# Kernel optimization log

Hardware: AMD Instinct MI355X
Metric: run time of the kernel (lower is better)

The kernel has to match this reference:

```python
import jax, jax.numpy as jnp
import numpy as np

D_MODEL = 2048
N_HEADS = 16
D_HEAD = 128
B = 2
S = 2048


def setup_inputs() -> dict:
    key = jax.random.key(0)
    ks = jax.random.split(key, 9)
    sc_in = 1.0 / np.sqrt(D_MODEL)
    sc_hd = 1.0 / np.sqrt(N_HEADS * D_HEAD)
    return {
        "x": jax.random.normal(ks[0], (B, S, D_MODEL), dtype=jnp.float32),
        "Wq": jax.random.normal(ks[1], (D_MODEL, N_HEADS * D_HEAD), dtype=jnp.float32) * sc_in,
        "bq": jax.random.normal(ks[2], (N_HEADS * D_HEAD,), dtype=jnp.float32) * 0.01,
        "Wk": jax.random.normal(ks[3], (D_MODEL, N_HEADS * D_HEAD), dtype=jnp.float32) * sc_in,
        "bk": jax.random.normal(ks[4], (N_HEADS * D_HEAD,), dtype=jnp.float32) * 0.01,
        "Wv": jax.random.normal(ks[5], (D_MODEL, N_HEADS * D_HEAD), dtype=jnp.float32) * sc_in,
        "bv": jax.random.normal(ks[6], (N_HEADS * D_HEAD,), dtype=jnp.float32) * 0.01,
        "Wo": jax.random.normal(ks[7], (N_HEADS * D_HEAD, D_MODEL), dtype=jnp.float32) * sc_hd,
        "bo": jax.random.normal(ks[8], (D_MODEL,), dtype=jnp.float32) * 0.01,
    }


def reference(x, Wq, bq, Wk, bk, Wv, bv, Wo, bo):
    b, s, _ = x.shape
    # projections -> [b, s, h, d] -> [b, h, s, d]
    q = (x @ Wq + bq).reshape(b, s, N_HEADS, D_HEAD).transpose(0, 2, 1, 3)
    k = (x @ Wk + bk).reshape(b, s, N_HEADS, D_HEAD).transpose(0, 2, 1, 3)
    v = (x @ Wv + bv).reshape(b, s, N_HEADS, D_HEAD).transpose(0, 2, 1, 3)
    scale = 1.0 / jnp.sqrt(jnp.asarray(D_HEAD, dtype=x.dtype))
    scores = jnp.einsum("bhsd,bhtd->bhst", q, k) * scale  # [b,h,s,s]
    causal = jnp.triu(jnp.ones((s, s), dtype=bool), k=1)
    scores = jnp.where(causal, jnp.asarray(-jnp.inf, dtype=scores.dtype), scores)
    attn = jax.nn.softmax(scores, axis=-1)
    ctx = jnp.einsum("bhst,bhtd->bhsd", attn, v)  # [b,h,s,d]
    ctx = ctx.transpose(0, 2, 1, 3).reshape(b, s, N_HEADS * D_HEAD)
    return ctx @ Wo + bo
```

## Files before the change

kernel.cpp:

```cpp
#include <hip/hip_runtime.h>
#include <hip/hip_bf16.h>
#include <stdint.h>

#define S_LEN  2048
#define DMODEL 2048
#define NHEADS 16
#define DHEAD  128
#define NBATCH 2
#define MROWS  (NBATCH * S_LEN)

typedef __bf16 bf16_t;
typedef __bf16 bf16x8 __attribute__((ext_vector_type(8)));
typedef float  f32x4  __attribute__((ext_vector_type(4)));
typedef float  f32x16 __attribute__((ext_vector_type(16)));

#define MFMA_BF16(A, B, C) __builtin_amdgcn_mfma_f32_16x16x32_bf16((A), (B), (C), 0, 0, 0)
#define MFMA32(A, B, C)    __builtin_amdgcn_mfma_f32_32x32x16_bf16((A), (B), (C), 0, 0, 0)

__device__ __forceinline__ void gload_lds16(const void* g, void* l) {
  __builtin_amdgcn_global_load_lds(
      (__attribute__((address_space(1))) uint32_t*)(uintptr_t)g,
      (__attribute__((address_space(3))) uint32_t*)l,
      16, 0, 0);
}

__device__ __forceinline__ unsigned pk2(float lo, float hi) {
  const unsigned short a = __builtin_bit_cast(unsigned short, (bf16_t)lo);
  const unsigned short b = __builtin_bit_cast(unsigned short, (bf16_t)hi);
  return (unsigned)a | ((unsigned)b << 16);
}

__global__ __launch_bounds__(256) void cast_kernel(const float* __restrict__ X,
                                                   bf16_t* __restrict__ Xb) {
  const int i = blockIdx.x * 256 + threadIdx.x;
  const f32x4 a = ((const f32x4*)X)[2 * i];
  const f32x4 b = ((const f32x4*)X)[2 * i + 1];
  bf16x8 o;
#pragma unroll
  for (int j = 0; j < 4; ++j) { o[j] = (bf16_t)a[j]; o[j + 4] = (bf16_t)b[j]; }
  ((bf16x8*)Xb)[i] = o;
}

__global__ __launch_bounds__(256) void transpose_cast(
    const float* __restrict__ W0, const float* __restrict__ W1,
    const float* __restrict__ W2, const float* __restrict__ W3,
    bf16_t* __restrict__ T0, bf16_t* __restrict__ T1,
    bf16_t* __restrict__ T2, bf16_t* __restrict__ T3) {
  const float* W; bf16_t* T;
  switch (blockIdx.z) {
    case 0:  W = W0; T = T0; break;
    case 1:  W = W1; T = T1; break;
    case 2:  W = W2; T = T2; break;
    default: W = W3; T = T3; break;
  }
  __shared__ float tile[64][65];
  const int r0 = blockIdx.y * 64;
  const int c0 = blockIdx.x * 64;
  const int tx = threadIdx.x & 63;
  const int ty = threadIdx.x >> 6;
#pragma unroll
  for (int i = 0; i < 16; ++i) {
    const int r = ty + i * 4;
    tile[r][tx] = W[(size_t)(r0 + r) * DMODEL + c0 + tx];
  }
  __syncthreads();
#pragma unroll
  for (int i = 0; i < 16; ++i) {
    const int r = ty + i * 4;
    T[(size_t)(c0 + r) * DMODEL + r0 + tx] = (bf16_t)tile[tx][r];
  }
}

__global__ __launch_bounds__(256) void transpose_v(const bf16_t* __restrict__ V,
                                                   bf16_t* __restrict__ VT) {
  __shared__ bf16_t tile[64 * 64];
  const int bh = blockIdx.z;
  const int s0 = blockIdx.x * 64;
  const int d0 = blockIdx.y * 64;
  const bf16_t* src = V + ((size_t)bh * S_LEN + s0) * DHEAD + d0;
#pragma unroll
  for (int i = 0; i < 2; ++i) {
    const int v = threadIdx.x + i * 256;
    const int r = v >> 3, ch = v & 7;
    *(bf16x8*)&tile[r * 64 + ((ch ^ ((r >> 3) & 7)) << 3)] =
        *(const bf16x8*)(src + (size_t)r * DHEAD + ch * 8);
  }
  __syncthreads();
  bf16_t* dst = VT + ((size_t)bh * DHEAD + d0) * S_LEN + s0;
#pragma unroll
  for (int i = 0; i < 2; ++i) {
    const int v = threadIdx.x + i * 256;
    const int d = v >> 3, j = v & 7;
    bf16x8 o;
#pragma unroll
    for (int e = 0; e < 8; ++e) {
      const int row = j * 8 + e;
      o[e] = tile[row * 64 + (((d >> 3) ^ j) << 3) + (d & 7)];
    }
    *(bf16x8*)(dst + (size_t)d * S_LEN + j * 8) = o;
  }
}

__global__ __launch_bounds__(512, 2) void gemm_qkv(
    const bf16_t* __restrict__ Xb,
    const bf16_t* __restrict__ WqT, const bf16_t* __restrict__ WkT,
    const bf16_t* __restrict__ WvT,
    const float* __restrict__ bq, const float* __restrict__ bk,
    const float* __restrict__ bv,
    bf16_t* __restrict__ Qg, bf16_t* __restrict__ Kg, bf16_t* __restrict__ Vg) {
  __shared__ __align__(16) char lds[2 * 65536];

  const int tid  = threadIdx.x;
  const int lane = tid & 63;
  const int w    = tid >> 6;
  const int g    = lane >> 4;
  const int l16  = lane & 15;
  const int wm   = w >> 2;
  const int wn   = w & 3;
  const int NTILES = DMODEL / 64;

  const int bid = blockIdx.x;
  const int wg  = (bid & 7) * 48 + (bid >> 3);
  const int mi  = wg / 24;
  const int ni  = wg % 24;
  const int z0  = ni >> 3;
  const bf16_t* Bt = (z0 == 0) ? WqT : (z0 == 1) ? WkT : WvT;
  const bf16_t* Abase = Xb + (size_t)mi * 256 * DMODEL;
  const bf16_t* Bbase = Bt + (size_t)(ni & 7) * 256 * DMODEL;

  f32x4 acc[8][4];
#pragma unroll
  for (int i = 0; i < 8; ++i)
#pragma unroll
    for (int j = 0; j < 4; ++j) acc[i][j] = (f32x4){0.f, 0.f, 0.f, 0.f};

  auto stage = [&](int tile, int mat, int half) {
    if (tile >= NTILES) return;
    const bf16_t* gb = (mat ? Bbase : Abase) + (size_t)(half * 128) * DMODEL + tile * 64;
    char* unit = lds + (tile & 1) * 65536 + mat * 32768 + half * 16384;
#pragma unroll
    for (int jj = 0; jj < 2; ++jj) {
      const int c   = jj * 512 + tid;
      const int row = c >> 3;
      const int ch  = c & 7;
      gload_lds16(gb + (size_t)row * DMODEL + ((ch ^ (row & 7)) << 3),
                  unit + (jj * 512 + (tid & ~63)) * 16);
    }
  };

  stage(0, 0, 0); stage(0, 0, 1); stage(0, 1, 0); stage(0, 1, 1);
  stage(1, 0, 0); stage(1, 0, 1);
  asm volatile("s_waitcnt vmcnt(4)" ::: "memory");
  __builtin_amdgcn_s_barrier();

  for (int t = 0; t < NTILES; ++t) {
    const char* cbA = lds + (t & 1) * 65536;
    const char* cbB = cbA + 32768;
    bf16x8 af[4][2], bf0[2][2], bf1[2][2];

#pragma unroll
    for (int i = 0; i < 4; ++i) {
      const int row = wm * 128 + i * 16 + l16;
#pragma unroll
      for (int ks = 0; ks < 2; ++ks)
        af[i][ks] = *(const bf16x8*)(cbA + row * 128 + ((((ks << 2) | g) ^ (row & 7)) << 4));
    }
#pragma unroll
    for (int j = 0; j < 2; ++j) {
      const int row = wn * 64 + j * 16 + l16;
#pragma unroll
      for (int ks = 0; ks < 2; ++ks)
        bf0[j][ks] = *(const bf16x8*)(cbB + row * 128 + ((((ks << 2) | g) ^ (row & 7)) << 4));
    }
    stage(t + 1, 1, 0);
    __builtin_amdgcn_s_barrier();
    asm volatile("s_waitcnt lgkmcnt(0)" ::: "memory");
    __builtin_amdgcn_s_setprio(1);
#pragma unroll
    for (int i = 0; i < 4; ++i)
#pragma unroll
      for (int j = 0; j < 2; ++j) {
        acc[i][j] = MFMA_BF16(af[i][0], bf0[j][0], acc[i][j]);
        acc[i][j] = MFMA_BF16(af[i][1], bf0[j][1], acc[i][j]);
      }
    __builtin_amdgcn_s_setprio(0);
    __builtin_amdgcn_s_barrier();

#pragma unroll
    for (int j = 0; j < 2; ++j) {
      const int row = wn * 64 + (j + 2) * 16 + l16;
#pragma unroll
      for (int ks = 0; ks < 2; ++ks)
        bf1[j][ks] = *(const bf16x8*)(cbB + row * 128 + ((((ks << 2) | g) ^ (row & 7)) << 4));
    }
    stage(t + 1, 1, 1);
    __builtin_amdgcn_s_barrier();
    asm volatile("s_waitcnt lgkmcnt(0)" ::: "memory");
    __builtin_amdgcn_s_setprio(1);
#pragma unroll
    for (int i = 0; i < 4; ++i)
#pragma unroll
      for (int j = 0; j < 2; ++j) {
        acc[i][j + 2] = MFMA_BF16(af[i][0], bf1[j][0], acc[i][j + 2]);
        acc[i][j + 2] = MFMA_BF16(af[i][1], bf1[j][1], acc[i][j + 2]);
      }
    __builtin_amdgcn_s_setprio(0);
    __builtin_amdgcn_s_barrier();

#pragma unroll
    for (int i = 0; i < 4; ++i) {
      const int row = wm * 128 + (i + 4) * 16 + l16;
#pragma unroll
      for (int ks = 0; ks < 2; ++ks)
        af[i][ks] = *(const bf16x8*)(cbA + row * 128 + ((((ks << 2) | g) ^ (row & 7)) << 4));
    }
    __builtin_amdgcn_s_barrier();
    asm volatile("s_waitcnt lgkmcnt(0)" ::: "memory");
    __builtin_amdgcn_s_setprio(1);
#pragma unroll
    for (int i = 0; i < 4; ++i)
#pragma unroll
      for (int j = 0; j < 2; ++j) {
        acc[i + 4][j + 2] = MFMA_BF16(af[i][0], bf1[j][0], acc[i + 4][j + 2]);
        acc[i + 4][j + 2] = MFMA_BF16(af[i][1], bf1[j][1], acc[i + 4][j + 2]);
      }
    __builtin_amdgcn_s_setprio(0);
    __builtin_amdgcn_s_barrier();

    stage(t + 2, 0, 0); stage(t + 2, 0, 1);
    __builtin_amdgcn_s_setprio(1);
#pragma unroll
    for (int i = 0; i < 4; ++i)
#pragma unroll
      for (int j = 0; j < 2; ++j) {
        acc[i + 4][j] = MFMA_BF16(af[i][0], bf0[j][0], acc[i + 4][j]);
        acc[i + 4][j] = MFMA_BF16(af[i][1], bf0[j][1], acc[i + 4][j]);
      }
    __builtin_amdgcn_s_setprio(0);
    if (t < NTILES - 2) { asm volatile("s_waitcnt vmcnt(4)" ::: "memory"); }
    else                { asm volatile("s_waitcnt vmcnt(0)" ::: "memory"); }
    __builtin_amdgcn_s_barrier();
  }

  const float* bias = (z0 == 0) ? bq : (z0 == 1) ? bk : bv;
  bf16_t* outb      = (z0 == 0) ? Qg : (z0 == 1) ? Kg : Vg;
#pragma unroll
  for (int i = 0; i < 8; ++i) {
#pragma unroll
    for (int j = 0; j < 4; ++j) {
      const int nloc = (ni & 7) * 256 + wn * 64 + j * 16 + l16;
      const float bb = bias[nloc];
      const int h = nloc >> 7, d = nloc & (DHEAD - 1);
#pragma unroll
      for (int r = 0; r < 4; ++r) {
        const int mrow = mi * 256 + wm * 128 + i * 16 + g * 4 + r;
        const int b = mrow >> 11, s = mrow & (S_LEN - 1);
        outb[((size_t)(b * NHEADS + h) * S_LEN + s) * DHEAD + d] =
            (bf16_t)(acc[i][j][r] + bb);
      }
    }
  }
}

template <int MODE>
__device__ __forceinline__ void gemm8_body(const bf16_t* __restrict__ A,
                                           const bf16_t* __restrict__ Bt,
                                           const float* __restrict__ bias,
                                           void* __restrict__ out) {
  __shared__ __align__(16) char lds8[2 * 49152];
  const int tid  = threadIdx.x;
  const int lane = tid & 63;
  const int w    = tid >> 6;
  const int g    = lane >> 4;
  const int l16  = lane & 15;
  const int wm   = w >> 2;
  const int wn   = w & 3;
  const int m0   = blockIdx.y * 128;
  const int n0   = blockIdx.x * 256;

  f32x4 acc[4][4];
#pragma unroll
  for (int i = 0; i < 4; ++i)
#pragma unroll
    for (int j = 0; j < 4; ++j) acc[i][j] = (f32x4){0.f, 0.f, 0.f, 0.f};

  const int st_r0 = tid >> 3;
  const int st_ch = tid & 7;

  auto stage = [&](int tile, int r) {
    if (tile >= DMODEL / 64) return;
    const int kt = tile << 6;
    char* db = lds8 + (tile & 1) * 49152 + r * 16384 + w * 1024;
    const bf16_t* sb = (r == 0) ? (A + (size_t)m0 * DMODEL + kt)
                                : (Bt + (size_t)(n0 + ((r - 1) << 7)) * DMODEL + kt);
#pragma unroll
    for (int jj = 0; jj < 2; ++jj) {
      const int row = jj * 64 + st_r0;
      gload_lds16(sb + (size_t)row * DMODEL + ((st_ch ^ (row & 7)) << 3),
                  db + jj * 8192);
    }
  };

  stage(0, 0); stage(0, 1); stage(0, 2); stage(1, 0);
  asm volatile("s_waitcnt vmcnt(2)" ::: "memory");
  __builtin_amdgcn_s_barrier();

#pragma unroll 2
  for (int t = 0; t < DMODEL / 64; ++t) {
    const char* cb = lds8 + (t & 1) * 49152;
    bf16x8 af[4][2], b0[2][2], b1[2][2];
#pragma unroll
    for (int i = 0; i < 4; ++i) {
      const int row = wm * 64 + i * 16 + l16;
      const char* rp = cb + row * 128;
#pragma unroll
      for (int ks = 0; ks < 2; ++ks)
        af[i][ks] = *(const bf16x8*)(rp + ((((ks << 2) | g) ^ (row & 7)) << 4));
    }
#pragma unroll
    for (int j = 0; j < 2; ++j) {
      const int row = (wn & 1) * 64 + j * 16 + l16;
      const char* rp = cb + 16384 + (wn >> 1) * 16384 + row * 128;
#pragma unroll
      for (int ks = 0; ks < 2; ++ks)
        b0[j][ks] = *(const bf16x8*)(rp + ((((ks << 2) | g) ^ (row & 7)) << 4));
    }
    stage(t + 1, 1); stage(t + 1, 2);
    __builtin_amdgcn_s_barrier();
    asm volatile("s_waitcnt lgkmcnt(0)" ::: "memory");
    __builtin_amdgcn_s_setprio(1);
#pragma unroll
    for (int i = 0; i < 4; ++i)
#pragma unroll
      for (int j = 0; j < 2; ++j) {
        acc[i][j] = MFMA_BF16(af[i][0], b0[j][0], acc[i][j]);
        acc[i][j] = MFMA_BF16(af[i][1], b0[j][1], acc[i][j]);
      }
    __builtin_amdgcn_s_setprio(0);
    __builtin_amdgcn_s_barrier();
#pragma unroll
    for (int j = 0; j < 2; ++j) {
      const int row = (wn & 1) * 64 + (j + 2) * 16 + l16;
      const char* rp = cb + 16384 + (wn >> 1) * 16384 + row * 128;
#pragma unroll
      for (int ks = 0; ks < 2; ++ks)
        b1[j][ks] = *(const bf16x8*)(rp + ((((ks << 2) | g) ^ (row & 7)) << 4));
    }
    stage(t + 2, 0);
    __builtin_amdgcn_s_barrier();
    asm volatile("s_waitcnt lgkmcnt(0)" ::: "memory");
    __builtin_amdgcn_s_setprio(1);
#pragma unroll
    for (int i = 0; i < 4; ++i)
#pragma unroll
      for (int j = 0; j < 2; ++j) {
        acc[i][j + 2] = MFMA_BF16(af[i][0], b1[j][0], acc[i][j + 2]);
        acc[i][j + 2] = MFMA_BF16(af[i][1], b1[j][1], acc[i][j + 2]);
      }
    __builtin_amdgcn_s_setprio(0);
    if (t < DMODEL / 64 - 2) asm volatile("s_waitcnt vmcnt(2)" ::: "memory");
    else                     asm volatile("s_waitcnt vmcnt(0)" ::: "memory");
    __builtin_amdgcn_s_barrier();
  }

#pragma unroll
  for (int i = 0; i < 4; ++i) {
#pragma unroll
    for (int j = 0; j < 4; ++j) {
      const int n    = n0 + wn * 64 + j * 16 + l16;
      const float bb = bias[n];
#pragma unroll
      for (int r = 0; r < 4; ++r) {
        const int m   = m0 + wm * 64 + i * 16 + g * 4 + r;
        const float v = acc[i][j][r] + bb;
        if (MODE == 0) {
          const int b = m >> 11, s = m & (S_LEN - 1);
          const int h = n >> 7,  d = n & (DHEAD - 1);
          ((bf16_t*)out)[((size_t)(b * NHEADS + h) * S_LEN + s) * DHEAD + d] = (bf16_t)v;
        } else {
          ((float*)out)[(size_t)m * DMODEL + n] = v;
        }
      }
    }
  }
}

__global__ __launch_bounds__(512, 2) void gemm_out(
    const bf16_t* __restrict__ Ctx, const bf16_t* __restrict__ WoT,
    const float* __restrict__ bo, float* __restrict__ out) {
  gemm8_body<1>(Ctx, WoT, bo, out);
}

#define KLDS_BYTES (64 * 272)
#define VLDS_BYTES (128 * 144)
#define BUF_BYTES  (KLDS_BYTES + VLDS_BYTES)

__global__ __launch_bounds__(256, 2) void attn_kernel(
    const bf16_t* __restrict__ Qg, const bf16_t* __restrict__ Kg,
    const bf16_t* __restrict__ VTg, bf16_t* __restrict__ ctx) {
  __shared__ __align__(16) char ldsbuf[2][BUF_BYTES];
  __shared__ float lbuf[4][32];

  const int tid  = threadIdx.x;
  const int lane = tid & 63;
  const int w    = tid >> 6;
  const int l31  = lane & 31;
  const int hi   = lane >> 5;

  const int id   = blockIdx.x;
  const int bh   = id & 31;
  const int jraw = id >> 5;
  const int j    = (jraw < 8) ? jraw : 23 - jraw;
  const int q0   = j * 128;
  const int qw   = q0 + w * 32;
  const int tq   = (qw + 31) >> 6;
  const int NT   = (q0 + 128) >> 6;

  const size_t bho = (size_t)bh * S_LEN * DHEAD;
  const bf16_t* Qb  = Qg + bho;
  const bf16_t* Kb  = Kg + bho;
  const bf16_t* VTb = VTg + bho;

  bf16x8 qreg[8];
#pragma unroll
  for (int s = 0; s < 8; ++s)
    qreg[s] = *(const bf16x8*)(Qb + (size_t)(qw + l31) * DHEAD + s * 16 + hi * 8);

  f32x16 oacc[4];
#pragma unroll
  for (int d0 = 0; d0 < 4; ++d0)
#pragma unroll
    for (int e = 0; e < 16; ++e) oacc[d0][e] = 0.f;

  float m = -1e30f, lsum = 0.f;
  const float sc2 = 0.12751751135f;

  bf16x8 kst[4], vst[4];
#pragma unroll
  for (int i = 0; i < 4; ++i) {
    const int c = tid + i * 256;
    kst[i] = *(const bf16x8*)(Kb + (size_t)(c >> 4) * DHEAD + (c & 15) * 8);
    vst[i] = *(const bf16x8*)(VTb + (size_t)(c >> 3) * S_LEN + (c & 7) * 8);
  }
#pragma unroll
  for (int i = 0; i < 4; ++i) {
    const int c  = tid + i * 256;
    const int kr = c >> 4, kc = c & 15;
    *(bf16x8*)(ldsbuf[0] + kr * 272 + ((kc ^ ((kr >> 3) & 3)) << 4)) = kst[i];
    const int vr = c >> 3, vc = c & 7;
    *(bf16x8*)(ldsbuf[0] + KLDS_BYTES + vr * 144 + ((vc ^ ((vr >> 3) & 3)) << 4)) = vst[i];
  }
  __syncthreads();

  for (int t = 0; t < NT; ++t) {
    const int kt = t << 6;
    const char* bK = ldsbuf[t & 1];
    const char* bV = bK + KLDS_BYTES;
    const bool hn = (t + 1 < NT);
    if (hn) {
#pragma unroll
      for (int i = 0; i < 4; ++i) {
        const int c = tid + i * 256;
        kst[i] = *(const bf16x8*)(Kb + (size_t)(kt + 64 + (c >> 4)) * DHEAD + (c & 15) * 8);
        vst[i] = *(const bf16x8*)(VTb + (size_t)(c >> 3) * S_LEN + kt + 64 + (c & 7) * 8);
      }
    }

    if (t <= tq) {
      f32x16 stt[2];
#pragma unroll
      for (int kh = 0; kh < 2; ++kh)
#pragma unroll
        for (int e = 0; e < 16; ++e) stt[kh][e] = 0.f;
#pragma unroll
      for (int kh = 0; kh < 2; ++kh) {
        const int row = kh * 32 + l31;
        const char* rb = bK + row * 272;
        const int swz = ((row >> 3) & 3) << 4;
#pragma unroll
        for (int s = 0; s < 8; ++s) {
          const bf16x8 kf = *(const bf16x8*)(rb + ((((s << 1) | hi) << 4) ^ swz));
          stt[kh] = MFMA32(kf, qreg[s], stt[kh]);
        }
      }
      if (t == tq) {
        const int qg = qw + l31;
#pragma unroll
        for (int kh = 0; kh < 2; ++kh)
#pragma unroll
          for (int r = 0; r < 16; ++r) {
            const int kv = kt + kh * 32 + (r & 3) + 8 * (r >> 2) + 4 * hi;
            stt[kh][r] = (kv > qg) ? -1e30f : stt[kh][r];
          }
      }
      float pm = stt[0][0];
#pragma unroll
      for (int kh = 0; kh < 2; ++kh)
#pragma unroll
        for (int r = 0; r < 16; ++r)
          if (kh | r) pm = fmaxf(pm, stt[kh][r]);
      pm = fmaxf(pm, __shfl_xor(pm, 32));
      const float pmax = pm * sc2;
      if (!__all(pmax <= m + 8.f)) {
        const float mn   = fmaxf(m, pmax);
        const float corr = __builtin_amdgcn_exp2f(m - mn);
        m = mn;
        lsum *= corr;
        if (!hi) lbuf[w][l31] = corr;
#pragma unroll
        for (int r = 0; r < 16; ++r) {
          const float cr = lbuf[w][(r & 3) + 8 * (r >> 2) + 4 * hi];
#pragma unroll
          for (int d0 = 0; d0 < 4; ++d0) oacc[d0][r] *= cr;
        }
      }
      float rs = 0.f;
#pragma unroll
      for (int kh = 0; kh < 2; ++kh)
#pragma unroll
        for (int r = 0; r < 16; ++r) {
          const float p = __builtin_amdgcn_exp2f(__builtin_fmaf(stt[kh][r], sc2, -m));
          stt[kh][r] = p;
          rs += p;
        }
      rs += __shfl_xor(rs, 32);
      lsum += rs;
      unsigned pw_[2][8];
#pragma unroll
      for (int kh = 0; kh < 2; ++kh)
#pragma unroll
        for (int jj = 0; jj < 8; ++jj)
          pw_[kh][jj] = pk2(stt[kh][2 * jj], stt[kh][2 * jj + 1]);
      bf16x8 pa[4];
#pragma unroll
      for (int kh = 0; kh < 2; ++kh)
#pragma unroll
        for (int c2 = 0; c2 < 2; ++c2) {
          const unsigned o0 = pw_[kh][4 * c2 + 0], o1 = pw_[kh][4 * c2 + 1];
          const unsigned o2 = pw_[kh][4 * c2 + 2], o3 = pw_[kh][4 * c2 + 3];
          const unsigned p0 = (unsigned)__shfl_xor((int)o0, 32);
          const unsigned p1 = (unsigned)__shfl_xor((int)o1, 32);
          const unsigned p2 = (unsigned)__shfl_xor((int)o2, 32);
          const unsigned p3 = (unsigned)__shfl_xor((int)o3, 32);
          union { unsigned u[4]; bf16x8 v; } uu;
          uu.u[0] = hi ? p2 : o0;
          uu.u[1] = hi ? p3 : o1;
          uu.u[2] = hi ? o2 : p0;
          uu.u[3] = hi ? o3 : p1;
          pa[2 * kh + c2] = uu.v;
        }
#pragma unroll
      for (int d0 = 0; d0 < 4; ++d0) {
        const int row = d0 * 32 + l31;
        const char* rb = bV + row * 144;
        const int swz = ((row >> 3) & 3) << 4;
#pragma unroll
        for (int ks = 0; ks < 4; ++ks) {
          const bf16x8 vb = *(const bf16x8*)(rb + ((((ks << 1) | hi) << 4) ^ swz));
          oacc[d0] = MFMA32(pa[ks], vb, oacc[d0]);
        }
      }
    }
    __syncthreads();
    if (hn) {
      char* nB = ldsbuf[(t + 1) & 1];
#pragma unroll
      for (int i = 0; i < 4; ++i) {
        const int c  = tid + i * 256;
        const int kr = c >> 4, kc = c & 15;
        *(bf16x8*)(nB + kr * 272 + ((kc ^ ((kr >> 3) & 3)) << 4)) = kst[i];
        const int vr = c >> 3, vc = c & 7;
        *(bf16x8*)(nB + KLDS_BYTES + vr * 144 + ((vc ^ ((vr >> 3) & 3)) << 4)) = vst[i];
      }
    }
    __syncthreads();
  }

  if (!hi) lbuf[w][l31] = 1.0f / lsum;
  const int b = bh >> 4, h = bh & 15;
#pragma unroll
  for (int r = 0; r < 16; ++r) {
    const int cro = (r & 3) + 8 * (r >> 2) + 4 * hi;
    const float li = lbuf[w][cro];
    const size_t base = ((size_t)(b * S_LEN + qw + cro)) * DMODEL + h * DHEAD;
#pragma unroll
    for (int d0 = 0; d0 < 4; ++d0)
      ctx[base + d0 * 32 + l31] = (bf16_t)(oacc[d0][r] * li);
  }
}

extern "C" void kernel_launch(void* const* d_in, const int* in_sizes, int n_in,
                              void* d_out, int out_size, void* d_ws, size_t ws_size,
                              hipStream_t stream) {
  const float* x  = (const float*)d_in[0];
  const float* Wq = (const float*)d_in[1];
  const float* bq = (const float*)d_in[2];
  const float* Wk = (const float*)d_in[3];
  const float* bk = (const float*)d_in[4];
  const float* Wv = (const float*)d_in[5];
  const float* bv = (const float*)d_in[6];
  const float* Wo = (const float*)d_in[7];
  const float* bo = (const float*)d_in[8];

  char* ws = (char*)d_ws;
  const size_t MB = 1ull << 20;
  bf16_t* Xb  = (bf16_t*)(ws + 0);
  bf16_t* VTg = (bf16_t*)(ws + 0);
  bf16_t* WqT = (bf16_t*)(ws + 16 * MB);
  bf16_t* WkT = (bf16_t*)(ws + 24 * MB);
  bf16_t* WvT = (bf16_t*)(ws + 32 * MB);
  bf16_t* WoT = (bf16_t*)(ws + 40 * MB);
  bf16_t* Qg  = (bf16_t*)(ws + 48 * MB);
  bf16_t* Kg  = (bf16_t*)(ws + 64 * MB);
  bf16_t* Vg  = (bf16_t*)(ws + 80 * MB);
  bf16_t* Ctx = (bf16_t*)(ws + 96 * MB);
  if (ws_size < 112 * MB) return;

  cast_kernel<<<dim3(MROWS * DMODEL / (256 * 8)), 256, 0, stream>>>(x, Xb);
  transpose_cast<<<dim3(32, 32, 4), 256, 0, stream>>>(Wq, Wk, Wv, Wo, WqT, WkT, WvT, WoT);
  gemm_qkv<<<dim3(384), 512, 0, stream>>>(
      Xb, WqT, WkT, WvT, bq, bk, bv, Qg, Kg, Vg);
  transpose_v<<<dim3(32, 2, 32), 256, 0, stream>>>(Vg, VTg);
  attn_kernel<<<dim3(512), 256, 0, stream>>>(Qg, Kg, VTg, Ctx);
  gemm_out<<<dim3(DMODEL / 256, MROWS / 128), 512, 0, stream>>>(Ctx, WoT, bo, (float*)d_out);
}
```

Measured before the change: 245.6 us.

## Stage attention K/V via direct global-to-LDS loads and reorder QKV GEMM staging

The attention kernel now copies K and V^T tiles straight from global memory into LDS with global_load_lds, using an XOR swizzle on unpadded rows. This replaces the register-staged loads and the second LDS store pass, and drops one barrier per iteration. The QKV GEMM changes which half-tiles are prefetched at each sub-phase: B is staged two tiles ahead and A one ahead, and the last two MFMA blocks swap order. Risks are LDS bank conflicts from the new swizzle and the vmcnt(0) wait each iteration, which may expose load latency.

Measured after the change: 240.1 us. 1.02x faster.

```diff
diff --git a/kernel.cpp b/kernel.cpp
--- a/kernel.cpp
+++ b/kernel.cpp
@@ -108,7 +108,7 @@
     const float* __restrict__ bq, const float* __restrict__ bk,
     const float* __restrict__ bv,
     bf16_t* __restrict__ Qg, bf16_t* __restrict__ Kg, bf16_t* __restrict__ Vg) {
-  __shared__ __align__(16) char lds[2 * 65536];
+  __shared__ __align__(16) char lds[2][65536];
 
   const int tid  = threadIdx.x;
   const int lane = tid & 63;
@@ -117,7 +117,7 @@
   const int l16  = lane & 15;
   const int wm   = w >> 2;
   const int wn   = w & 3;
-  const int NTILES = DMODEL / 64;
+  const int NT   = DMODEL / 64;
 
   const int bid = blockIdx.x;
   const int wg  = (bid & 7) * 48 + (bid >> 3);
@@ -135,9 +135,9 @@
     for (int j = 0; j < 4; ++j) acc[i][j] = (f32x4){0.f, 0.f, 0.f, 0.f};
 
   auto stage = [&](int tile, int mat, int half) {
-    if (tile >= NTILES) return;
+    if (tile >= NT) return;
     const bf16_t* gb = (mat ? Bbase : Abase) + (size_t)(half * 128) * DMODEL + tile * 64;
-    char* unit = lds + (tile & 1) * 65536 + mat * 32768 + half * 16384;
+    char* unit = &lds[tile & 1][0] + mat * 32768 + half * 16384;
 #pragma unroll
     for (int jj = 0; jj < 2; ++jj) {
       const int c   = jj * 512 + tid;
@@ -149,30 +149,32 @@
   };
 
   stage(0, 0, 0); stage(0, 0, 1); stage(0, 1, 0); stage(0, 1, 1);
-  stage(1, 0, 0); stage(1, 0, 1);
+  stage(1, 1, 0); stage(1, 1, 1);
   asm volatile("s_waitcnt vmcnt(4)" ::: "memory");
   __builtin_amdgcn_s_barrier();
 
-  for (int t = 0; t < NTILES; ++t) {
-    const char* cbA = lds + (t & 1) * 65536;
-    const char* cbB = cbA + 32768;
-    bf16x8 af[4][2], bf0[2][2], bf1[2][2];
+  bf16x8 af[4][2], bn0[2][2], bn1[2][2];
+  for (int t = 0; t < NT; ++t) {
+    const char* bufA = &lds[t & 1][0] + wm * 16384;
+    const char* bufB = &lds[t & 1][0] + 32768 + (wn >> 1) * 16384;
 
 #pragma unroll
     for (int i = 0; i < 4; ++i) {
-      const int row = wm * 128 + i * 16 + l16;
+      const int row = i * 16 + l16;
+      const char* rp = bufA + row * 128;
 #pragma unroll
       for (int ks = 0; ks < 2; ++ks)
-        af[i][ks] = *(const bf16x8*)(cbA + row * 128 + ((((ks << 2) | g) ^ (row & 7)) << 4));
+        af[i][ks] = *(const bf16x8*)(rp + ((((ks << 2) | g) ^ (row & 7)) << 4));
     }
 #pragma unroll
     for (int j = 0; j < 2; ++j) {
-      const int row = wn * 64 + j * 16 + l16;
+      const int row = (wn & 1) * 64 + j * 16 + l16;
+      const char* rp = bufB + row * 128;
 #pragma unroll
       for (int ks = 0; ks < 2; ++ks)
-        bf0[j][ks] = *(const bf16x8*)(cbB + row * 128 + ((((ks << 2) | g) ^ (row & 7)) << 4));
-    }
-    stage(t + 1, 1, 0);
+        bn0[j][ks] = *(const bf16x8*)(rp + ((((ks << 2) | g) ^ (row & 7)) << 4));
+    }
+    stage(t + 1, 0, 0);
     __builtin_amdgcn_s_barrier();
     asm volatile("s_waitcnt lgkmcnt(0)" ::: "memory");
     __builtin_amdgcn_s_setprio(1);
@@ -180,20 +182,21 @@
     for (int i = 0; i < 4; ++i)
 #pragma unroll
       for (int j = 0; j < 2; ++j) {
-        acc[i][j] = MFMA_BF16(af[i][0], bf0[j][0], acc[i][j]);
-        acc[i][j] = MFMA_BF16(af[i][1], bf0[j][1], acc[i][j]);
+        acc[i][j] = MFMA_BF16(af[i][0], bn0[j][0], acc[i][j]);
+        acc[i][j] = MFMA_BF16(af[i][1], bn0[j][1], acc[i][j]);
       }
     __builtin_amdgcn_s_setprio(0);
     __builtin_amdgcn_s_barrier();
 
 #pragma unroll
     for (int j = 0; j < 2; ++j) {
-      const int row = wn * 64 + (j + 2) * 16 + l16;
+      const int row = (wn & 1) * 64 + 32 + j * 16 + l16;
+      const char* rp = bufB + row * 128;
 #pragma unroll
       for (int ks = 0; ks < 2; ++ks)
-        bf1[j][ks] = *(const bf16x8*)(cbB + row * 128 + ((((ks << 2) | g) ^ (row & 7)) << 4));
-    }
-    stage(t + 1, 1, 1);
+        bn1[j][ks] = *(const bf16x8*)(rp + ((((ks << 2) | g) ^ (row & 7)) << 4));
+    }
+    stage(t + 1, 0, 1);
     __builtin_amdgcn_s_barrier();
     asm volatile("s_waitcnt lgkmcnt(0)" ::: "memory");
     __builtin_amdgcn_s_setprio(1);
@@ -201,19 +204,21 @@
     for (int i = 0; i < 4; ++i)
 #pragma unroll
       for (int j = 0; j < 2; ++j) {
-        acc[i][j + 2] = MFMA_BF16(af[i][0], bf1[j][0], acc[i][j + 2]);
-        acc[i][j + 2] = MFMA_BF16(af[i][1], bf1[j][1], acc[i][j + 2]);
+        acc[i][j + 2] = MFMA_BF16(af[i][0], bn1[j][0], acc[i][j + 2]);
+        acc[i][j + 2] = MFMA_BF16(af[i][1], bn1[j][1], acc[i][j + 2]);
       }
     __builtin_amdgcn_s_setprio(0);
     __builtin_amdgcn_s_barrier();
 
 #pragma unroll
     for (int i = 0; i < 4; ++i) {
-      const int row = wm * 128 + (i + 4) * 16 + l16;
+      const int row = 64 + i * 16 + l16;
+      const char* rp = bufA + row * 128;
 #pragma unroll
       for (int ks = 0; ks < 2; ++ks)
-        af[i][ks] = *(const bf16x8*)(cbA + row * 128 + ((((ks << 2) | g) ^ (row & 7)) << 4));
-    }
+        af[i][ks] = *(const bf16x8*)(rp + ((((ks << 2) | g) ^ (row & 7)) << 4));
+    }
+    stage(t + 2, 1, 0);
     __builtin_amdgcn_s_barrier();
     asm volatile("s_waitcnt lgkmcnt(0)" ::: "memory");
     __builtin_amdgcn_s_setprio(1);
@@ -221,24 +226,24 @@
     for (int i = 0; i < 4; ++i)
 #pragma unroll
       for (int j = 0; j < 2; ++j) {
-        acc[i + 4][j + 2] = MFMA_BF16(af[i][0], bf1[j][0], acc[i + 4][j + 2]);
-        acc[i + 4][j + 2] = MFMA_BF16(af[i][1], bf1[j][1], acc[i + 4][j + 2]);
+        acc[i + 4][j] = MFMA_BF16(af[i][0], bn0[j][0], acc[i + 4][j]);
+        acc[i + 4][j] = MFMA_BF16(af[i][1], bn0[j][1], acc[i + 4][j]);
       }
     __builtin_amdgcn_s_setprio(0);
     __builtin_amdgcn_s_barrier();
 
-    stage(t + 2, 0, 0); stage(t + 2, 0, 1);
+    stage(t + 2, 1, 1);
     __builtin_amdgcn_s_setprio(1);
 #pragma unroll
     for (int i = 0; i < 4; ++i)
 #pragma unroll
       for (int j = 0; j < 2; ++j) {
-        acc[i + 4][j] = MFMA_BF16(af[i][0], bf0[j][0], acc[i + 4][j]);
-        acc[i + 4][j] = MFMA_BF16(af[i][1], bf0[j][1], acc[i + 4][j]);
+        acc[i + 4][j + 2] = MFMA_BF16(af[i][0], bn1[j][0], acc[i + 4][j + 2]);
+        acc[i + 4][j + 2] = MFMA_BF16(af[i][1], bn1[j][1], acc[i + 4][j + 2]);
       }
     __builtin_amdgcn_s_setprio(0);
-    if (t < NTILES - 2) { asm volatile("s_waitcnt vmcnt(4)" ::: "memory"); }
-    else                { asm volatile("s_waitcnt vmcnt(0)" ::: "memory"); }
+    if (t < NT - 2) asm volatile("s_waitcnt vmcnt(4)" ::: "memory");
+    else            asm volatile("s_waitcnt vmcnt(0)" ::: "memory");
     __builtin_amdgcn_s_barrier();
   }
 
@@ -391,14 +396,14 @@
   gemm8_body<1>(Ctx, WoT, bo, out);
 }
 
-#define KLDS_BYTES (64 * 272)
-#define VLDS_BYTES (128 * 144)
-#define BUF_BYTES  (KLDS_BYTES + VLDS_BYTES)
+#define KTILE_B 16384
+#define VTILE_B 16384
+#define ABUF_B  (KTILE_B + VTILE_B)
 
 __global__ __launch_bounds__(256, 2) void attn_kernel(
     const bf16_t* __restrict__ Qg, const bf16_t* __restrict__ Kg,
     const bf16_t* __restrict__ VTg, bf16_t* __restrict__ ctx) {
-  __shared__ __align__(16) char ldsbuf[2][BUF_BYTES];
+  __shared__ __align__(16) char ldsbuf[2][ABUF_B];
   __shared__ float lbuf[4][32];
 
   const int tid  = threadIdx.x;
@@ -421,6 +426,25 @@
   const bf16_t* Kb  = Kg + bho;
   const bf16_t* VTb = VTg + bho;
 
+  auto stageT = [&](int t) {
+    const int kt = t << 6;
+    char* dst = ldsbuf[t & 1];
+#pragma unroll
+    for (int i = 0; i < 4; ++i) {
+      const int c   = i * 256 + tid;
+      const int row = c >> 4, ch = c & 15;
+      gload_lds16(Kb + (size_t)(kt + row) * DHEAD + ((ch ^ (row & 7)) << 3),
+                  dst + (i * 256 + (tid & ~63)) * 16);
+    }
+#pragma unroll
+    for (int i = 0; i < 4; ++i) {
+      const int c   = i * 256 + tid;
+      const int row = c >> 3, ch = c & 7;
+      gload_lds16(VTb + (size_t)row * S_LEN + kt + ((ch ^ (row & 7)) << 3),
+                  dst + KTILE_B + (i * 256 + (tid & ~63)) * 16);
+    }
+  };
+
   bf16x8 qreg[8];
 #pragma unroll
   for (int s = 0; s < 8; ++s)
@@ -435,38 +459,17 @@
   float m = -1e30f, lsum = 0.f;
   const float sc2 = 0.12751751135f;
 
-  bf16x8 kst[4], vst[4];
-#pragma unroll
-  for (int i = 0; i < 4; ++i) {
-    const int c = tid + i * 256;
-    kst[i] = *(const bf16x8*)(Kb + (size_t)(c >> 4) * DHEAD + (c & 15) * 8);
-    vst[i] = *(const bf16x8*)(VTb + (size_t)(c >> 3) * S_LEN + (c & 7) * 8);
-  }
-#pragma unroll
-  for (int i = 0; i < 4; ++i) {
-    const int c  = tid + i * 256;
-    const int kr = c >> 4, kc = c & 15;
-    *(bf16x8*)(ldsbuf[0] + kr * 272 + ((kc ^ ((kr >> 3) & 3)) << 4)) = kst[i];
-    const int vr = c >> 3, vc = c & 7;
-    *(bf16x8*)(ldsbuf[0] + KLDS_BYTES + vr * 144 + ((vc ^ ((vr >> 3) & 3)) << 4)) = vst[i];
-  }
+  stageT(0);
+  asm volatile("s_waitcnt vmcnt(0)" ::: "memory");
   __syncthreads();
 
   for (int t = 0; t < NT; ++t) {
-    const int kt = t << 6;
     const char* bK = ldsbuf[t & 1];
-    const char* bV = bK + KLDS_BYTES;
-    const bool hn = (t + 1 < NT);
-    if (hn) {
-#pragma unroll
-      for (int i = 0; i < 4; ++i) {
-        const int c = tid + i * 256;
-        kst[i] = *(const bf16x8*)(Kb + (size_t)(kt + 64 + (c >> 4)) * DHEAD + (c & 15) * 8);
-        vst[i] = *(const bf16x8*)(VTb + (size_t)(c >> 3) * S_LEN + kt + 64 + (c & 7) * 8);
-      }
-    }
+    const char* bV = bK + KTILE_B;
+    if (t + 1 < NT) stageT(t + 1);
 
     if (t <= tq) {
+      const int kt = t << 6;
       f32x16 stt[2];
 #pragma unroll
       for (int kh = 0; kh < 2; ++kh)
@@ -475,8 +478,8 @@
 #pragma unroll
       for (int kh = 0; kh < 2; ++kh) {
         const int row = kh * 32 + l31;
-        const char* rb = bK + row * 272;
-        const int swz = ((row >> 3) & 3) << 4;
+        const char* rb = bK + row * 256;
+        const int swz = (row & 7) << 4;
 #pragma unroll
         for (int s = 0; s < 8; ++s) {
           const bf16x8 kf = *(const bf16x8*)(rb + ((((s << 1) | hi) << 4) ^ swz));
@@ -552,8 +555,8 @@
 #pragma unroll
       for (int d0 = 0; d0 < 4; ++d0) {
         const int row = d0 * 32 + l31;
-        const char* rb = bV + row * 144;
-        const int swz = ((row >> 3) & 3) << 4;
+        const char* rb = bV + row * 128;
+        const int swz = (row & 7) << 4;
 #pragma unroll
         for (int ks = 0; ks < 4; ++ks) {
           const bf16x8 vb = *(const bf16x8*)(rb + ((((ks << 1) | hi) << 4) ^ swz));
@@ -561,18 +564,7 @@
         }
       }
     }
-    __syncthreads();
-    if (hn) {
-      char* nB = ldsbuf[(t + 1) & 1];
-#pragma unroll
-      for (int i = 0; i < 4; ++i) {
-        const int c  = tid + i * 256;
-        const int kr = c >> 4, kc = c & 15;
-        *(bf16x8*)(nB + kr * 272 + ((kc ^ ((kr >> 3) & 3)) << 4)) = kst[i];
-        const int vr = c >> 3, vc = c & 7;
-        *(bf16x8*)(nB + KLDS_BYTES + vr * 144 + ((vc ^ ((vr >> 3) & 3)) << 4)) = vst[i];
-      }
-    }
+    asm volatile("s_waitcnt vmcnt(0)" ::: "memory");
     __syncthreads();
   }
 
```
